# Performance work log

Hardware: AMD Instinct MI355X
Metric: run time of the kernel (lower is better)

## Reference

```python
import jax, jax.numpy as jnp
import numpy as np

B, N, D = 2, 128, 128          # batch, nodes, dim
DE = 64                        # dim_edge_refinement
H, DH = 8, 32                  # heads, per-head dim
DI = H * DH                    # dim_inner = dim * dim_head = 256
DMI = 2 * DI                   # mlp_expansion_factor * dim_inner = 512
MD = 2                         # max_degree
S = 1 + 2 * MD                 # value/edge channel groups = 5
FFD = 512                      # int(2.0 * dim * 2) for EquivariantFeedForward


def _ln(x, g, eps=1e-5):
    mu = x.mean(-1, keepdims=True)
    var = ((x - mu) ** 2).mean(-1, keepdims=True)
    return (x - mu) / jnp.sqrt(var + eps) * g


def setup_inputs() -> dict:
    key = jax.random.key(0)
    ks = iter(jax.random.split(key, 64))
    def rn(shape, scale=1.0):
        return jax.random.normal(next(ks), shape, dtype=jnp.float32) * scale
    w = 0.05
    return dict(
        h=rn((B, N, D)), x1=rn((B, N, D, 3)), x2=rn((B, N, D, 5)),
        t_ij=rn((B, N, N, D)), r1=rn((B, N, N, 3)), r2=rn((B, N, N, 5)),
        g_i=jnp.ones((D,), jnp.float32), g_j=jnp.ones((D,), jnp.float32),
        Wq=rn((D, DI), w), Wk=rn((D, DI), w),
        Wv1=rn((D, DMI), w), bv1=jnp.zeros((DMI,), jnp.float32),
        Wv2=rn((DMI, S * DI), w), bv2=jnp.zeros((S * DI,), jnp.float32),
        Wp1=rn((D, DMI), w), bp1=jnp.zeros((DMI,), jnp.float32),
        Wp2=rn((DMI, S * DI), w), bp2=jnp.zeros((S * DI,), jnp.float32),
        Wek=rn((D, S * DI), w), Wev=rn((D, S * DI), w),
        Wcomb=rn((DI, D), w),
        Wqh=rn((D, DE), w), Wk1h=rn((D, DE), w), Wk2h=rn((D, DE), w),
        Wep=rn((2 * DE, D), w), Wres=rn((D, D), w),
        P1=rn((D, D), w), P2=rn((D, D), w),
        Wf1a=rn((2 * D, FFD), w), bf1a=jnp.zeros((FFD,), jnp.float32),
        Wf2a=rn((FFD, 2 * D), w), bf2a=jnp.zeros((2 * D,), jnp.float32),
        Wf1b=rn((2 * D, FFD), w), bf1b=jnp.zeros((FFD,), jnp.float32),
        Wf2b=rn((FFD, 2 * D), w), bf2b=jnp.zeros((2 * D,), jnp.float32),
    )


def reference(h, x1, x2, t_ij, r1, r2, g_i, g_j, Wq, Wk, Wv1, bv1, Wv2, bv2,
              Wp1, bp1, Wp2, bp2, Wek, Wev, Wcomb, Wqh, Wk1h, Wk2h, Wep, Wres,
              P1, P2, Wf1a, bf1a, Wf2a, bf2a, Wf1b, bf1b, Wf2b, bf2b):
    # ---- HierarchicalTensorRefinement: per-degree inner products -> edge refresh
    q1 = jnp.einsum('bndm,de->bnem', x1, Wqh)
    q2 = jnp.einsum('bndm,de->bnem', x2, Wqh)
    k1 = jnp.einsum('bndm,de->bnem', x1, Wk1h)
    k2 = jnp.einsum('bndm,de->bnem', x2, Wk2h)
    w_ij = jnp.concatenate([
        jnp.einsum('biem,bjem->bije', q1, k1),
        jnp.einsum('biem,bjem->bije', q2, k2)], axis=-1)       # [b,n,n,2*DE]
    t = w_ij @ Wep + t_ij @ Wres                                # [b,n,n,D]
    # ---- GeometryAwareTensorAttention
    hi = _ln(h, g_i)
    hj = _ln(h, g_j)
    q = (hi @ Wq).reshape(B, N, H, DH).transpose(0, 2, 1, 3)    # bhnd
    k = (hj @ Wk).reshape(B, N, H, DH).transpose(0, 2, 1, 3)
    v = (jax.nn.silu(hj @ Wv1 + bv1) @ Wv2 + bv2).reshape(B, N, S, H, DH).transpose(0, 3, 1, 2, 4)   # bhnsd
    pv = (jax.nn.silu(hj @ Wp1 + bp1) @ Wp2 + bp2).reshape(B, N, S, H, DH).transpose(0, 3, 1, 2, 4)
    ek = jax.nn.silu(t @ Wek).reshape(B, N, N, S, H, DH).transpose(0, 4, 1, 2, 3, 5)                  # bhijsd
    ev = (t @ Wev).reshape(B, N, N, S, H, DH).transpose(0, 4, 1, 2, 3, 5)
    sim_num = jnp.einsum('bhid,bhjd->bhij', q, k)
    sim_den = jnp.einsum('bhid,bhijsd->bhis', q, ek)            # edge-keyed denominator
    attn = sim_num[..., None] / sim_den[:, :, :, None, :]       # bhijs
    sea = attn[..., None] * v[:, :, None] + ev * pv[:, :, None]  # bhijsd
    out = sea.transpose(0, 2, 3, 4, 1, 5).reshape(B, N, N, S, H * DH) @ Wcomb  # [b,i,j,S,D]
    h_sc = out[..., 0, :]              # [b,i,j,D]
    r_sc = out[..., 1:1 + MD, :]       # [b,i,j,MD,D]
    x_sc = out[..., 1 + MD:, :]        # [b,i,j,MD,D]
    h2 = h + h_sc.sum(axis=2)
    x1a = jnp.einsum('bjdm,bijd->bidm', x1, x_sc[..., 0, :]) + jnp.einsum('bijm,bijd->bidm', r1, r_sc[..., 0, :])
    x2a = jnp.einsum('bjdm,bijd->bidm', x2, x_sc[..., 1, :]) + jnp.einsum('bijm,bijd->bidm', r2, r_sc[..., 1, :])
    # ---- EquivariantFeedForward (eq 13)
    def ff_branch(xl, P, W1, b1, W2, b2):
        proj = jnp.einsum('bndm,de->bnem', xl, P)
        inv = jnp.sqrt((proj ** 2).sum(-1) + 1e-12)             # invariant norm over m
        mo = jax.nn.silu(jnp.concatenate([h2, inv], -1) @ W1 + b1) @ W2 + b2
        m1, m2 = jnp.split(mo, 2, axis=-1)
        return m1, proj * m2[..., None]
    m1a, xr1 = ff_branch(x1a, P1, Wf1a, bf1a, Wf2a, bf2a)
    m1b, xr2 = ff_branch(x2a, P2, Wf1b, bf1b, Wf2b, bf2b)
    h3 = h2 + m1a + m1b
    x1f = x1a + xr1
    x2f = x2a + xr2
    # pack outputs: h [b,n,d,1] | x1 [b,n,d,3] | x2 [b,n,d,5] -> [b,n,d,9]
    return jnp.concatenate([h3[..., None], x1f, x2f], axis=-1)
```

## Files before the change

### kernel.cpp

```cpp
#include <hip/hip_runtime.h>
#include <math.h>

#define OFF_Q    0
#define OFF_K    65536
#define OFF_A1V  131072
#define OFF_A1P  262144
#define OFF_V    393216
#define OFF_PV   720896
#define OFF_VW   1048576
#define OFF_QK   2359296
#define OFF_T    2621440
#define OFF_DEN  6815744
#define OFF_ACC  6825984
#define OFF_WEVT 7940096
#define OFF_WCT  8022016
#define OFF_HI   8038400
#define OFF_HJ   8071168

typedef __bf16 bf16x8 __attribute__((ext_vector_type(8)));
typedef float  f32x4  __attribute__((ext_vector_type(4)));

__device__ __forceinline__ float silu_f(float x){
  return x / (1.0f + __expf(-x));
}
__device__ __forceinline__ unsigned short f2bf(float x){
  union{float f; unsigned u;} c; c.f = x;
  unsigned r = c.u + 0x7FFFu + ((c.u >> 16) & 1u);
  return (unsigned short)(r >> 16);
}
__device__ __forceinline__ unsigned packbf(float a, float b){
  return (unsigned)f2bf(a) | ((unsigned)f2bf(b) << 16);
}
__device__ __forceinline__ void swz_store(float* Abase, int k, int j, float v){
  *(float*)((char*)Abase + k*256 + ((((j>>2) ^ ((k>>2)&15))) << 4) + ((j&3)<<2)) = v;
}
__device__ __forceinline__ f32x4 swz_load4(const float* Abase, int k, int chunk){
  return *(const f32x4*)((const char*)Abase + k*256 + ((chunk ^ ((k>>2)&15)) << 4));
}

__global__ __launch_bounds__(128) void k0a_ln(
    const float* __restrict__ h, const float* __restrict__ g_i, const float* __restrict__ g_j,
    float* __restrict__ ws)
{
  __shared__ float red[2];
  const int r = blockIdx.x, tid = threadIdx.x;
  const int w = tid >> 6, l = tid & 63;
  const float hv = h[r*128 + tid];
  float s = hv;
  #pragma unroll
  for (int o = 1; o < 64; o <<= 1) s += __shfl_xor(s, o);
  if (l == 0) red[w] = s;
  __syncthreads();
  const float mu = (red[0] + red[1]) * (1.f/128.f);
  const float dv = hv - mu;
  float s2 = dv*dv;
  #pragma unroll
  for (int o = 1; o < 64; o <<= 1) s2 += __shfl_xor(s2, o);
  __syncthreads();
  if (l == 0) red[w] = s2;
  __syncthreads();
  const float rstd = 1.0f / sqrtf((red[0] + red[1])*(1.f/128.f) + 1e-5f);
  ws[OFF_HI + r*128 + tid] = dv * rstd * g_i[tid];
  ws[OFF_HJ + r*128 + tid] = dv * rstd * g_j[tid];
  if (tid < 40) ws[OFF_DEN + r*40 + tid] = 0.f;
}

__global__ __launch_bounds__(256) void k0b_qkv(
    const float* __restrict__ Wq, const float* __restrict__ Wk,
    const float* __restrict__ Wv1, const float* __restrict__ bv1,
    const float* __restrict__ Wp1, const float* __restrict__ bp1,
    float* __restrict__ ws)
{
  __shared__ float hrow[128];
  const int bid = blockIdx.x;
  const int row = bid / 6, ch = bid - 6*(bid/6);
  const int tid = threadIdx.x;
  if (tid < 128) hrow[tid] = ws[((ch == 0) ? OFF_HI : OFF_HJ) + row*128 + tid];
  __syncthreads();
  const float* W; int c; float bias = 0.f; bool act = false; float* dst; int wstride;
  switch(ch){
    case 0: W = Wq;  c = tid;      wstride = 256; dst = ws + OFF_Q   + row*256 + c; break;
    case 1: W = Wk;  c = tid;      wstride = 256; dst = ws + OFF_K   + row*256 + c; break;
    case 2: W = Wv1; c = tid;      wstride = 512; bias = bv1[c]; act = true; dst = ws + OFF_A1V + row*512 + c; break;
    case 3: W = Wv1; c = 256+tid;  wstride = 512; bias = bv1[c]; act = true; dst = ws + OFF_A1V + row*512 + c; break;
    case 4: W = Wp1; c = tid;      wstride = 512; bias = bp1[c]; act = true; dst = ws + OFF_A1P + row*512 + c; break;
    default:W = Wp1; c = 256+tid;  wstride = 512; bias = bp1[c]; act = true; dst = ws + OFF_A1P + row*512 + c; break;
  }
  float acc = bias;
  #pragma unroll 8
  for (int d = 0; d < 128; ++d) acc += hrow[d] * W[d*wstride + c];
  *dst = act ? silu_f(acc) : acc;
}

__global__ __launch_bounds__(256) void k0c_qk12(
    const float* __restrict__ x1, const float* __restrict__ x2,
    const float* __restrict__ Wqh, const float* __restrict__ Wk1h, const float* __restrict__ Wk2h,
    float* __restrict__ ws)
{
  __shared__ float x1r[384], x2r[640];
  const int row = blockIdx.x, tid = threadIdx.x;
  for (int idx = tid; idx < 384; idx += 256) x1r[idx] = x1[row*384 + idx];
  for (int idx = tid; idx < 640; idx += 256) x2r[idx] = x2[row*640 + idx];
  __syncthreads();
  for (int idx = tid; idx < 512; idx += 256){
    if (idx < 192){
      const int e = idx/3, m = idx - e*3;
      float qa = 0.f, ka = 0.f;
      #pragma unroll 8
      for (int d = 0; d < 128; ++d){
        const float xv = x1r[d*3 + m];
        qa += xv*Wqh[d*64 + e];
        ka += xv*Wk1h[d*64 + e];
      }
      ws[OFF_QK + row*1024 + idx] = qa;
      ws[OFF_QK + row*1024 + 512 + idx] = ka;
    } else {
      const int i2 = idx - 192;
      const int e = i2/5, m = i2 - e*5;
      float qa = 0.f, ka = 0.f;
      #pragma unroll 8
      for (int d = 0; d < 128; ++d){
        const float xv = x2r[d*5 + m];
        qa += xv*Wqh[d*64 + e];
        ka += xv*Wk2h[d*64 + e];
      }
      ws[OFF_QK + row*1024 + 192 + i2] = qa;
      ws[OFF_QK + row*1024 + 704 + i2] = ka;
    }
  }
}

__global__ __launch_bounds__(256) void k1_vp(
    const float* __restrict__ Wv2, const float* __restrict__ bv2,
    const float* __restrict__ Wp2, const float* __restrict__ bp2,
    float* __restrict__ ws)
{
  __shared__ float A[512][16];
  __shared__ float Bc[64][128];
  const int tid = threadIdx.x;
  const int rt = blockIdx.x & 31;
  const int ct = blockIdx.x >> 5;
  const int r0 = rt*16;
  const bool isP = (r0 >= 256);
  const int rbase = isP ? (r0 - 256) : r0;
  const float* __restrict__ src  = ws + (isP ? OFF_A1P : OFF_A1V);
  const float* __restrict__ W    = isP ? Wp2 : Wv2;
  const float* __restrict__ bias = isP ? bp2 : bv2;
  const int c0 = ct*128;
  for (int idx = tid; idx < 2048; idx += 256){
    const int rl = idx & 15;
    const int c4 = (idx >> 4) * 4;
    const float4 v = *(const float4*)&src[(rbase+rl)*512 + c4];
    A[c4+0][rl] = v.x; A[c4+1][rl] = v.y; A[c4+2][rl] = v.z; A[c4+3][rl] = v.w;
  }
  float acc[4][2] = {{0.f}};
  const int rg = tid & 3;
  const int cg = tid >> 2;
  for (int kc = 0; kc < 8; ++kc){
    __syncthreads();
    for (int idx = tid; idx < 2048; idx += 256){
      const int kl = idx >> 5;
      const int c4 = (idx & 31)*4;
      *(float4*)&Bc[kl][c4] = *(const float4*)&W[(kc*64+kl)*1280 + c0 + c4];
    }
    __syncthreads();
    #pragma unroll 8
    for (int k = 0; k < 64; ++k){
      const float4 a = *(const float4*)&A[kc*64+k][rg*4];
      const float b0 = Bc[k][cg*2], b1 = Bc[k][cg*2+1];
      acc[0][0] += a.x*b0; acc[0][1] += a.x*b1;
      acc[1][0] += a.y*b0; acc[1][1] += a.y*b1;
      acc[2][0] += a.z*b0; acc[2][1] += a.z*b1;
      acc[3][0] += a.w*b0; acc[3][1] += a.w*b1;
    }
  }
  float* __restrict__ dst = ws + (isP ? OFF_PV : OFF_V);
  for (int rr = 0; rr < 4; ++rr)
    for (int cc = 0; cc < 2; ++cc){
      const int c = c0 + cg*2 + cc;
      dst[(rbase + rg*4 + rr)*1280 + c] = acc[rr][cc] + bias[c];
    }
}

__global__ __launch_bounds__(256) void k2_vw(const float* __restrict__ Wcomb, float* __restrict__ ws)
{
  __shared__ float vr[1280];
  const int j = blockIdx.x, tid = threadIdx.x;
  for (int idx = tid; idx < 320; idx += 256)
    *(float4*)&vr[idx*4] = *(const float4*)&ws[OFF_V + j*1280 + idx*4];
  __syncthreads();
  const int d = tid & 127;
  for (int sh = tid >> 7; sh < 40; sh += 2){
    const int s = sh >> 3, hh = sh & 7;
    float a = 0.f;
    #pragma unroll 8
    for (int dh = 0; dh < 32; ++dh)
      a += vr[s*256 + hh*32 + dh] * Wcomb[(hh*32+dh)*128 + d];
    ws[OFF_VW + j*5120 + sh*128 + d] = a;
  }
}

__global__ __launch_bounds__(256) void k_cvt(
    const float* __restrict__ Wev, const float* __restrict__ Wcomb, float* __restrict__ ws)
{
  __shared__ float ld[16][256];
  const int tid = threadIdx.x;
  if (blockIdx.x < 80){
    const int c0 = blockIdx.x*16;
    for (int p = 0; p < 8; ++p){
      const int idx = tid + p*256;
      const int k = idx >> 4, cl = idx & 15;
      ld[cl][k] = Wev[k*1280 + c0 + cl];
    }
    __syncthreads();
    const int cl = tid >> 4, k8 = tid & 15;
    uint4 u;
    u.x = packbf(ld[cl][k8*8+0], ld[cl][k8*8+1]);
    u.y = packbf(ld[cl][k8*8+2], ld[cl][k8*8+3]);
    u.z = packbf(ld[cl][k8*8+4], ld[cl][k8*8+5]);
    u.w = packbf(ld[cl][k8*8+6], ld[cl][k8*8+7]);
    ((uint4*)(ws + OFF_WEVT))[(c0+cl)*16 + k8] = u;
  } else {
    const int c0 = (blockIdx.x - 80)*16;
    for (int p = 0; p < 16; ++p){
      const int idx = tid + p*256;
      const int k = idx >> 4, cl = idx & 15;
      ld[cl][k] = Wcomb[k*128 + c0 + cl];
    }
    __syncthreads();
    const int cl = tid >> 4, k8i = tid & 15;
    for (int pass = 0; pass < 2; ++pass){
      const int k8 = k8i + pass*16;
      uint4 u;
      u.x = packbf(ld[cl][k8*8+0], ld[cl][k8*8+1]);
      u.y = packbf(ld[cl][k8*8+2], ld[cl][k8*8+3]);
      u.z = packbf(ld[cl][k8*8+4], ld[cl][k8*8+5]);
      u.w = packbf(ld[cl][k8*8+6], ld[cl][k8*8+7]);
      ((uint4*)(ws + OFF_WCT))[(c0+cl)*32 + k8] = u;
    }
  }
}

__global__ __launch_bounds__(512, 2) void k3_t(
    const float* __restrict__ t_ij, const float* __restrict__ Wep, const float* __restrict__ Wres,
    float* __restrict__ ws)
{
  __shared__ float A[16384];
  __shared__ float qrow[512];
  float* kst = A + 8192;
  const int tid = threadIdx.x;
  const int bi = blockIdx.x >> 1;
  const int jt = blockIdx.x & 1;
  const int j0 = jt*64;
  const int b  = bi >> 7;
  if (tid < 128) *(float4*)&qrow[tid*4] = *(const float4*)&ws[OFF_QK + bi*1024 + tid*4];
  for (int jq = 0; jq < 4; ++jq){
    __syncthreads();
    for (int idx = tid; idx < 2048; idx += 512){
      const int jl = idx & 15;
      const int c4 = (idx >> 4)*4;
      const float4 v = *(const float4*)&ws[OFF_QK + (b*128 + j0 + jq*16 + jl)*1024 + 512 + c4];
      kst[(c4+0)*16 + jl] = v.x; kst[(c4+1)*16 + jl] = v.y;
      kst[(c4+2)*16 + jl] = v.z; kst[(c4+3)*16 + jl] = v.w;
    }
    __syncthreads();
    for (int idx = tid; idx < 2048; idx += 512){
      const int jl = idx & 15;
      const int e  = idx >> 4;
      float acc = 0.f;
      if (e < 64){
        #pragma unroll
        for (int m = 0; m < 3; ++m) acc += qrow[e*3+m] * kst[(e*3+m)*16 + jl];
      } else {
        const int e2 = e - 64;
        #pragma unroll
        for (int m = 0; m < 5; ++m) acc += qrow[192 + e2*5+m] * kst[(192 + e2*5+m)*16 + jl];
      }
      swz_store(A, e, jq*16 + jl, acc);
    }
  }
  __syncthreads();
  for (int idx = tid; idx < 2048; idx += 512){
    const int jl = idx >> 5;
    const int d4 = (idx & 31)*4;
    const float4 v = *(const float4*)&t_ij[(bi*128 + j0 + jl)*128 + d4];
    swz_store(A, 128+d4+0, jl, v.x);
    swz_store(A, 128+d4+1, jl, v.y);
    swz_store(A, 128+d4+2, jl, v.z);
    swz_store(A, 128+d4+3, jl, v.w);
  }
  __syncthreads();
  const int jg = tid >> 5;
  const int cg = tid & 31;
  f32x4 acc[4] = {{0,0,0,0},{0,0,0,0},{0,0,0,0},{0,0,0,0}};
  {
    const float* Wp = Wep + cg*4;
    f32x4 wv = *(const f32x4*)Wp;
    for (int k = 0; k < 127; ++k){
      const f32x4 wn = *(const f32x4*)(Wp + (k+1)*128);
      const f32x4 av = swz_load4(A, k, jg);
      acc[0] += wv*av[0]; acc[1] += wv*av[1]; acc[2] += wv*av[2]; acc[3] += wv*av[3];
      wv = wn;
    }
    const f32x4 av = swz_load4(A, 127, jg);
    acc[0] += wv*av[0]; acc[1] += wv*av[1]; acc[2] += wv*av[2]; acc[3] += wv*av[3];
  }
  {
    const float* Wp = Wres + cg*4;
    f32x4 wv = *(const f32x4*)Wp;
    for (int k = 0; k < 127; ++k){
      const f32x4 wn = *(const f32x4*)(Wp + (k+1)*128);
      const f32x4 av = swz_load4(A, 128+k, jg);
      acc[0] += wv*av[0]; acc[1] += wv*av[1]; acc[2] += wv*av[2]; acc[3] += wv*av[3];
      wv = wn;
    }
    const f32x4 av = swz_load4(A, 255, jg);
    acc[0] += wv*av[0]; acc[1] += wv*av[1]; acc[2] += wv*av[2]; acc[3] += wv*av[3];
  }
  #pragma unroll
  for (int jj = 0; jj < 4; ++jj)
    *(f32x4*)&ws[OFF_T + (bi*128 + j0 + jg*4 + jj)*128 + cg*4] = acc[jj];
}

__global__ __launch_bounds__(256) void k4_den(
    const float* __restrict__ Wek, float* __restrict__ ws)
{
  __shared__ float tl[8192];
  __shared__ float colsum[8][128];
  __shared__ float den40[40];
  const int tid = threadIdx.x;
  const int bid = blockIdx.x;
  const int bi = bid / 20;
  const int rem = bid - bi*20;
  const int jh = rem & 1;
  const int cq = rem >> 1;
  const int j0 = jh*64;
  for (int idx = tid; idx < 2048; idx += 256){
    const int j = idx >> 5;
    const int d4 = (idx & 31)*4;
    const float4 v = *(const float4*)&ws[OFF_T + (bi*128 + j0 + j)*128 + d4];
    swz_store(tl, d4+0, j, v.x);
    swz_store(tl, d4+1, j, v.y);
    swz_store(tl, d4+2, j, v.z);
    swz_store(tl, d4+3, j, v.w);
  }
  if (tid < 40) den40[tid] = 0.f;
  __syncthreads();
  const int w = tid >> 5;
  const int lane = tid & 31;
  const float* wekp = Wek + cq*128 + lane*4;
  f32x4 acc[8];
  #pragma unroll
  for (int i = 0; i < 8; ++i) acc[i] = (f32x4){0,0,0,0};
  f32x4 wv = *(const f32x4*)wekp;
  for (int k = 0; k < 127; ++k){
    const f32x4 wn = *(const f32x4*)(wekp + (k+1)*1280);
    #pragma unroll
    for (int q = 0; q < 2; ++q){
      const f32x4 tv = swz_load4(tl, k, w*2 + q);
      acc[q*4+0] += wv*tv[0]; acc[q*4+1] += wv*tv[1];
      acc[q*4+2] += wv*tv[2]; acc[q*4+3] += wv*tv[3];
    }
    wv = wn;
  }
  #pragma unroll
  for (int q = 0; q < 2; ++q){
    const f32x4 tv = swz_load4(tl, 127, w*2 + q);
    acc[q*4+0] += wv*tv[0]; acc[q*4+1] += wv*tv[1];
    acc[q*4+2] += wv*tv[2]; acc[q*4+3] += wv*tv[3];
  }
  f32x4 cs = {0,0,0,0};
  #pragma unroll
  for (int i = 0; i < 8; ++i){
    #pragma unroll
    for (int cc = 0; cc < 4; ++cc) cs[cc] += silu_f(acc[i][cc]);
  }
  *(f32x4*)&colsum[w][lane*4] = cs;
  __syncthreads();
  if (tid < 128){
    const int c = tid;
    const float jsum = colsum[0][c] + colsum[1][c] + colsum[2][c] + colsum[3][c]
                     + colsum[4][c] + colsum[5][c] + colsum[6][c] + colsum[7][c];
    const int col = cq*128 + c;
    const int s  = col >> 8;
    const int hd = col & 255;
    atomicAdd(&den40[(hd>>5)*5 + s], jsum * ws[OFF_Q + bi*256 + hd]);
  }
  __syncthreads();
  if (tid < 40 && den40[tid] != 0.f)
    atomicAdd(&ws[OFF_DEN + bi*40 + tid], den40[tid]);
}

__global__ __launch_bounds__(512, 4) void k5_pass2(
    const float* __restrict__ x1, const float* __restrict__ x2,
    const float* __restrict__ r1, const float* __restrict__ r2,
    float* __restrict__ ws)
{
  __shared__ unsigned short tA[8192];
  __shared__ unsigned short wevB[8192];
  __shared__ unsigned short wcombB[8192];
  __shared__ unsigned short epB[4096];
  __shared__ float num[8][64];
  __shared__ float acc17[17*128];
  __shared__ float ql[256];
  __shared__ float rdenl[40];

  const int tid  = threadIdx.x;
  const int lane = tid & 63;
  const int w    = tid >> 6;
  const int wm   = w & 3;
  const int wn   = w >> 2;
  const int l15  = lane & 15;
  const int kq   = lane >> 4;

  const int bi = blockIdx.x >> 1;
  const int jh = blockIdx.x & 1;
  const int j0 = jh*64;
  const int b  = bi >> 7;

  #pragma unroll
  for (int p = 0; p < 4; ++p){
    const int idx = tid + p*512;
    const int j = idx >> 5;
    const int d4 = (idx & 31)*4;
    const float4 v = *(const float4*)&ws[OFF_T + (bi*128 + j0 + j)*128 + d4];
    uint2 u;
    u.x = packbf(v.x, v.y);
    u.y = packbf(v.z, v.w);
    *(uint2*)((char*)tA + j*256 + ((d4*2) ^ ((j&7)<<4))) = u;
  }
  if (tid < 64) *(float4*)&ql[tid*4] = *(const float4*)&ws[OFF_Q + bi*256 + tid*4];
  if (tid < 40) rdenl[tid] = 1.0f / ws[OFF_DEN + bi*40 + tid];
  for (int idx = tid; idx < 17*128; idx += 512) acc17[idx] = 0.f;
  __syncthreads();

  {
    const int hh = tid >> 6, jl = tid & 63;
    const float* krow = &ws[OFF_K + (b*128 + j0 + jl)*256 + hh*32];
    float a = 0.f;
    #pragma unroll
    for (int dh = 0; dh < 32; ++dh) a += ql[hh*32+dh]*krow[dh];
    num[hh][jl] = a;
  }

  const int jA = wm*16 + l15;
  bf16x8 af[4];
  #pragma unroll
  for (int ks = 0; ks < 4; ++ks)
    af[ks] = *(const bf16x8*)((const char*)tA + jA*256 + ((ks*64 + kq*16) ^ ((jA&7)<<4)));

  const uint4* wevt = (const uint4*)(ws + OFF_WEVT);
  const uint4* wct  = (const uint4*)(ws + OFF_WCT);

  for (int s = 0; s < 5; ++s){
    f32x4 o0 = {0,0,0,0}, o1 = {0,0,0,0}, o2 = {0,0,0,0}, o3 = {0,0,0,0};
    for (int ch4 = 0; ch4 < 4; ++ch4){
      __syncthreads();
      #pragma unroll
      for (int p = 0; p < 2; ++p){
        const int idx = tid + p*512;
        const int cl = idx & 63, kg = idx >> 6;
        const uint4 v = wevt[(s*256 + ch4*64 + cl)*16 + kg];
        *(uint4*)((char*)wevB + cl*256 + ((kg*16) ^ ((cl&7)<<4))) = v;
      }
      #pragma unroll
      for (int p = 0; p < 2; ++p){
        const int idx = tid + p*512;
        const int hg = idx & 7, d = idx >> 3;
        const uint4 v = wct[d*32 + ch4*8 + hg];
        *(uint4*)((char*)wcombB + d*128 + ((hg*16) ^ ((d&7)<<4))) = v;
      }
      __syncthreads();
      f32x4 ev0 = {0,0,0,0}, ev1 = {0,0,0,0};
      {
        const int c0l = wn*32 + l15;
        const int c1l = c0l + 16;
        #pragma unroll
        for (int ks = 0; ks < 4; ++ks){
          const bf16x8 b0 = *(const bf16x8*)((const char*)wevB + c0l*256 + ((ks*64 + kq*16) ^ ((c0l&7)<<4)));
          const bf16x8 b1 = *(const bf16x8*)((const char*)wevB + c1l*256 + ((ks*64 + kq*16) ^ ((c1l&7)<<4)));
          ev0 = __builtin_amdgcn_mfma_f32_16x16x32_bf16(af[ks], b0, ev0, 0, 0, 0);
          ev1 = __builtin_amdgcn_mfma_f32_16x16x32_bf16(af[ks], b1, ev1, 0, 0, 0);
        }
      }
      #pragma unroll
      for (int nt = 0; nt < 2; ++nt){
        const int cl = wn*32 + nt*16 + l15;
        const int cglob = s*256 + ch4*64 + cl;
        #pragma unroll
        for (int r = 0; r < 4; ++r){
          const int jl = wm*16 + kq*4 + r;
          const float pvv = ws[OFF_PV + (b*128 + j0 + jl)*1280 + cglob];
          const float evv = (nt == 0) ? ev0[r] : ev1[r];
          *(unsigned short*)((char*)epB + jl*128 + ((cl*2) ^ ((jl&7)<<4))) = f2bf(evv * pvv);
        }
      }
      __syncthreads();
      #pragma unroll
      for (int ks = 0; ks < 2; ++ks){
        const bf16x8 a = *(const bf16x8*)((const char*)epB + jA*128 + ((ks*64 + kq*16) ^ ((jA&7)<<4)));
        #pragma unroll
        for (int nt = 0; nt < 4; ++nt){
          const int dl = wn*64 + nt*16 + l15;
          const bf16x8 bb = *(const bf16x8*)((const char*)wcombB + dl*128 + ((ks*64 + kq*16) ^ ((dl&7)<<4)));
          if      (nt == 0) o0 = __builtin_amdgcn_mfma_f32_16x16x32_bf16(a, bb, o0, 0, 0, 0);
          else if (nt == 1) o1 = __builtin_amdgcn_mfma_f32_16x16x32_bf16(a, bb, o1, 0, 0, 0);
          else if (nt == 2) o2 = __builtin_amdgcn_mfma_f32_16x16x32_bf16(a, bb, o2, 0, 0, 0);
          else              o3 = __builtin_amdgcn_mfma_f32_16x16x32_bf16(a, bb, o3, 0, 0, 0);
        }
      }
    }
    #pragma unroll
    for (int r = 0; r < 4; ++r){
      const int jl = wm*16 + kq*4 + r;
      const float* vwbase = ws + OFF_VW + (b*128 + j0 + jl)*5120 + s*1024 + wn*64 + l15;
      #pragma unroll
      for (int hh = 0; hh < 8; ++hh){
        const float at = num[hh][jl] * rdenl[hh*5 + s];
        const float* vp = vwbase + hh*128;
        o0[r] += at * vp[0];
        o1[r] += at * vp[16];
        o2[r] += at * vp[32];
        o3[r] += at * vp[48];
      }
    }
    if (s == 0){
      #pragma unroll
      for (int nt = 0; nt < 4; ++nt){
        const f32x4 oo = (nt==0)?o0:(nt==1)?o1:(nt==2)?o2:o3;
        float p = oo[0] + oo[1] + oo[2] + oo[3];
        p += __shfl_xor(p, 16);
        p += __shfl_xor(p, 32);
        if (lane < 16) atomicAdd(&acc17[wn*64 + nt*16 + lane], p);
      }
    } else if (s <= 2){
      const int M = (s == 1) ? 3 : 5;
      const int slot0 = (s == 1) ? 1 : 4;
      const float* rw = (s == 1) ? r1 : r2;
      for (int m = 0; m < M; ++m){
        float wj[4];
        #pragma unroll
        for (int r = 0; r < 4; ++r)
          wj[r] = rw[(bi*128 + j0 + wm*16 + kq*4 + r)*M + m];
        #pragma unroll
        for (int nt = 0; nt < 4; ++nt){
          const f32x4 oo = (nt==0)?o0:(nt==1)?o1:(nt==2)?o2:o3;
          float p = wj[0]*oo[0] + wj[1]*oo[1] + wj[2]*oo[2] + wj[3]*oo[3];
          p += __shfl_xor(p, 16);
          p += __shfl_xor(p, 32);
          if (lane < 16) atomicAdd(&acc17[(slot0+m)*128 + wn*64 + nt*16 + lane], p);
        }
      }
    } else {
      const int M = (s == 3) ? 3 : 5;
      const int slot0 = (s == 3) ? 9 : 12;
      const float* xw = (s == 3) ? x1 : x2;
      for (int m = 0; m < M; ++m){
        #pragma unroll
        for (int nt = 0; nt < 4; ++nt){
          const int d = wn*64 + nt*16 + l15;
          const f32x4 oo = (nt==0)?o0:(nt==1)?o1:(nt==2)?o2:o3;
          float p = 0.f;
          #pragma unroll
          for (int r = 0; r < 4; ++r)
            p += xw[((b*128 + j0 + wm*16 + kq*4 + r)*128 + d)*M + m] * oo[r];
          p += __shfl_xor(p, 16);
          p += __shfl_xor(p, 32);
          if (lane < 16) atomicAdd(&acc17[(slot0+m)*128 + d], p);
        }
      }
    }
  }
  __syncthreads();
  for (int idx = tid; idx < 2176; idx += 512)
    ws[OFF_ACC + (bi*2 + jh)*2176 + idx] = acc17[idx];
}

__global__ __launch_bounds__(256) void k6_tail(
    const float* __restrict__ h,
    const float* __restrict__ P1, const float* __restrict__ P2,
    const float* __restrict__ Wf1a, const float* __restrict__ bf1a,
    const float* __restrict__ Wf2a, const float* __restrict__ bf2a,
    const float* __restrict__ Wf1b, const float* __restrict__ bf1b,
    const float* __restrict__ Wf2b, const float* __restrict__ bf2b,
    const float* __restrict__ ws, float* __restrict__ out)
{
  __shared__ float a17[2176];
  __shared__ float h2s[128];
  __shared__ float x1a[384], x2a[640];
  __shared__ float pj1[384], pj2[640];
  __shared__ float inv1[128], inv2[128];
  __shared__ float za[512], zb[512];
  __shared__ float m1a[128], m2a[128], m1b[128], m2b[128];
  const int tid = threadIdx.x;
  const int row = blockIdx.x;
  for (int idx = tid; idx < 2176; idx += 256)
    a17[idx] = ws[OFF_ACC + (row*2)*2176 + idx] + ws[OFF_ACC + (row*2+1)*2176 + idx];
  __syncthreads();
  if (tid < 128) h2s[tid] = h[row*128 + tid] + a17[tid];
  for (int idx = tid; idx < 384; idx += 256){
    const int d = idx/3, m = idx - d*3;
    x1a[idx] = a17[(1+m)*128 + d] + a17[(9+m)*128 + d];
  }
  for (int idx = tid; idx < 640; idx += 256){
    const int d = idx/5, m = idx - d*5;
    x2a[idx] = a17[(4+m)*128 + d] + a17[(12+m)*128 + d];
  }
  __syncthreads();
  if (tid < 128){
    const int e = tid;
    float pa[3] = {0.f,0.f,0.f};
    for (int d = 0; d < 128; ++d){
      const float p = P1[d*128 + e];
      pa[0] += x1a[d*3+0]*p;
      pa[1] += x1a[d*3+1]*p;
      pa[2] += x1a[d*3+2]*p;
    }
    pj1[e*3+0] = pa[0]; pj1[e*3+1] = pa[1]; pj1[e*3+2] = pa[2];
    inv1[e] = sqrtf(pa[0]*pa[0] + pa[1]*pa[1] + pa[2]*pa[2] + 1e-12f);
  } else {
    const int e = tid - 128;
    float pa[5] = {0.f,0.f,0.f,0.f,0.f};
    for (int d = 0; d < 128; ++d){
      const float p = P2[d*128 + e];
      pa[0] += x2a[d*5+0]*p;
      pa[1] += x2a[d*5+1]*p;
      pa[2] += x2a[d*5+2]*p;
      pa[3] += x2a[d*5+3]*p;
      pa[4] += x2a[d*5+4]*p;
    }
    #pragma unroll
    for (int m = 0; m < 5; ++m) pj2[e*5+m] = pa[m];
    inv2[e] = sqrtf(pa[0]*pa[0]+pa[1]*pa[1]+pa[2]*pa[2]+pa[3]*pa[3]+pa[4]*pa[4] + 1e-12f);
  }
  __syncthreads();
  for (int it = 0; it < 2; ++it){
    const int f = tid + it*256;
    float av = bf1a[f], bv_ = bf1b[f];
    #pragma unroll 4
    for (int k = 0; k < 128; ++k){
      av  += h2s[k]*Wf1a[k*512 + f];
      bv_ += h2s[k]*Wf1b[k*512 + f];
    }
    #pragma unroll 4
    for (int k = 0; k < 128; ++k){
      av  += inv1[k]*Wf1a[(128+k)*512 + f];
      bv_ += inv2[k]*Wf1b[(128+k)*512 + f];
    }
    za[f] = silu_f(av); zb[f] = silu_f(bv_);
  }
  __syncthreads();
  {
    const int g = tid;
    float am = bf2a[g], bm = bf2b[g];
    #pragma unroll 4
    for (int f = 0; f < 512; ++f){
      am += za[f]*Wf2a[f*256 + g];
      bm += zb[f]*Wf2b[f*256 + g];
    }
    if (g < 128){ m1a[g] = am; m1b[g] = bm; }
    else        { m2a[g-128] = am; m2b[g-128] = bm; }
  }
  __syncthreads();
  if (tid < 128){
    const int d = tid;
    const int ob = (row*128 + d)*9;
    out[ob+0] = h2s[d] + m1a[d] + m1b[d];
    #pragma unroll
    for (int m = 0; m < 3; ++m)
      out[ob+1+m] = x1a[d*3+m] + pj1[d*3+m]*m2a[d];
    #pragma unroll
    for (int m = 0; m < 5; ++m)
      out[ob+4+m] = x2a[d*5+m] + pj2[d*5+m]*m2b[d];
  }
}

extern "C" void kernel_launch(void* const* d_in, const int* in_sizes, int n_in,
                              void* d_out, int out_size, void* d_ws, size_t ws_size,
                              hipStream_t stream)
{
  (void)in_sizes; (void)n_in; (void)out_size; (void)ws_size;
  const float* h    = (const float*)d_in[0];
  const float* x1   = (const float*)d_in[1];
  const float* x2   = (const float*)d_in[2];
  const float* t_ij = (const float*)d_in[3];
  const float* r1   = (const float*)d_in[4];
  const float* r2   = (const float*)d_in[5];
  const float* g_i  = (const float*)d_in[6];
  const float* g_j  = (const float*)d_in[7];
  const float* Wq   = (const float*)d_in[8];
  const float* Wk   = (const float*)d_in[9];
  const float* Wv1  = (const float*)d_in[10];
  const float* bv1  = (const float*)d_in[11];
  const float* Wv2  = (const float*)d_in[12];
  const float* bv2  = (const float*)d_in[13];
  const float* Wp1  = (const float*)d_in[14];
  const float* bp1  = (const float*)d_in[15];
  const float* Wp2  = (const float*)d_in[16];
  const float* bp2  = (const float*)d_in[17];
  const float* Wek  = (const float*)d_in[18];
  const float* Wev  = (const float*)d_in[19];
  const float* Wcomb= (const float*)d_in[20];
  const float* Wqh  = (const float*)d_in[21];
  const float* Wk1h = (const float*)d_in[22];
  const float* Wk2h = (const float*)d_in[23];
  const float* Wep  = (const float*)d_in[24];
  const float* Wres = (const float*)d_in[25];
  const float* P1   = (const float*)d_in[26];
  const float* P2   = (const float*)d_in[27];
  const float* Wf1a = (const float*)d_in[28];
  const float* bf1a = (const float*)d_in[29];
  const float* Wf2a = (const float*)d_in[30];
  const float* bf2a = (const float*)d_in[31];
  const float* Wf1b = (const float*)d_in[32];
  const float* bf1b = (const float*)d_in[33];
  const float* Wf2b = (const float*)d_in[34];
  const float* bf2b = (const float*)d_in[35];
  float* ws  = (float*)d_ws;
  float* out = (float*)d_out;

  k0a_ln <<<dim3(256),  dim3(128), 0, stream>>>(h, g_i, g_j, ws);
  k0b_qkv<<<dim3(1536), dim3(256), 0, stream>>>(Wq, Wk, Wv1, bv1, Wp1, bp1, ws);
  k0c_qk12<<<dim3(256), dim3(256), 0, stream>>>(x1, x2, Wqh, Wk1h, Wk2h, ws);
  k1_vp  <<<dim3(320),  dim3(256), 0, stream>>>(Wv2, bv2, Wp2, bp2, ws);
  k2_vw  <<<dim3(256),  dim3(256), 0, stream>>>(Wcomb, ws);
  k_cvt  <<<dim3(88),   dim3(256), 0, stream>>>(Wev, Wcomb, ws);
  k3_t   <<<dim3(512),  dim3(512), 0, stream>>>(t_ij, Wep, Wres, ws);
  k4_den <<<dim3(5120), dim3(256), 0, stream>>>(Wek, ws);
  k5_pass2<<<dim3(512), dim3(512), 0, stream>>>(x1, x2, r1, r2, ws);
  k6_tail<<<dim3(256),  dim3(256), 0, stream>>>(h, P1, P2, Wf1a, bf1a, Wf2a, bf2a, Wf1b, bf1b, Wf2b, bf2b, ws, out);
}
```

Before: 702.1 us.

## Load MFMA operands directly from global memory and double-buffer epB in k5_pass2

k5_pass2 no longer stages t_ij, Wev^T and Wcomb^T tiles in LDS. A fragments are loaded and packed to bf16 straight from global memory into registers, and B fragments are read directly from the global bf16 weight buffers. The epB scratch is double-buffered so one barrier per chunk can be dropped, and the occupancy hint in launch_bounds is removed. This cuts LDS use and synchronisation, but depends on L1/L2 serving repeated, less coalesced global weight reads in place of LDS reuse.

Result: slower. 717.5 us (+2.2%).

```diff
diff --git a/kernel.cpp b/kernel.cpp
--- a/kernel.cpp
+++ b/kernel.cpp
@@ -391,15 +391,12 @@
     atomicAdd(&ws[OFF_DEN + bi*40 + tid], den40[tid]);
 }
 
-__global__ __launch_bounds__(512, 4) void k5_pass2(
+__global__ __launch_bounds__(512) void k5_pass2(
     const float* __restrict__ x1, const float* __restrict__ x2,
     const float* __restrict__ r1, const float* __restrict__ r2,
     float* __restrict__ ws)
 {
-  __shared__ unsigned short tA[8192];
-  __shared__ unsigned short wevB[8192];
-  __shared__ unsigned short wcombB[8192];
-  __shared__ unsigned short epB[4096];
+  __shared__ unsigned short epB[2][4096];
   __shared__ float num[8][64];
   __shared__ float acc17[17*128];
   __shared__ float ql[256];
@@ -418,20 +415,22 @@
   const int j0 = jh*64;
   const int b  = bi >> 7;
 
-  #pragma unroll
-  for (int p = 0; p < 4; ++p){
-    const int idx = tid + p*512;
-    const int j = idx >> 5;
-    const int d4 = (idx & 31)*4;
-    const float4 v = *(const float4*)&ws[OFF_T + (bi*128 + j0 + j)*128 + d4];
-    uint2 u;
-    u.x = packbf(v.x, v.y);
-    u.y = packbf(v.z, v.w);
-    *(uint2*)((char*)tA + j*256 + ((d4*2) ^ ((j&7)<<4))) = u;
-  }
   if (tid < 64) *(float4*)&ql[tid*4] = *(const float4*)&ws[OFF_Q + bi*256 + tid*4];
   if (tid < 40) rdenl[tid] = 1.0f / ws[OFF_DEN + bi*40 + tid];
   for (int idx = tid; idx < 17*128; idx += 512) acc17[idx] = 0.f;
+
+  const int jA = wm*16 + l15;
+  union { bf16x8 v; uint4 q; } afu[4];
+  #pragma unroll
+  for (int ks = 0; ks < 4; ++ks){
+    const float* tp = &ws[OFF_T + (bi*128 + j0 + jA)*128 + ks*32 + kq*8];
+    const float4 t0 = *(const float4*)tp;
+    const float4 t1 = *(const float4*)(tp + 4);
+    afu[ks].q.x = packbf(t0.x, t0.y);
+    afu[ks].q.y = packbf(t0.z, t0.w);
+    afu[ks].q.z = packbf(t1.x, t1.y);
+    afu[ks].q.w = packbf(t1.z, t1.w);
+  }
   __syncthreads();
 
   {
@@ -443,72 +442,53 @@
     num[hh][jl] = a;
   }
 
-  const int jA = wm*16 + l15;
-  bf16x8 af[4];
-  #pragma unroll
-  for (int ks = 0; ks < 4; ++ks)
-    af[ks] = *(const bf16x8*)((const char*)tA + jA*256 + ((ks*64 + kq*16) ^ ((jA&7)<<4)));
-
-  const uint4* wevt = (const uint4*)(ws + OFF_WEVT);
-  const uint4* wct  = (const uint4*)(ws + OFF_WCT);
-
+  const __bf16* wevt = (const __bf16*)(ws + OFF_WEVT);
+  const __bf16* wct  = (const __bf16*)(ws + OFF_WCT);
+
+  int pb = 0;
   for (int s = 0; s < 5; ++s){
     f32x4 o0 = {0,0,0,0}, o1 = {0,0,0,0}, o2 = {0,0,0,0}, o3 = {0,0,0,0};
     for (int ch4 = 0; ch4 < 4; ++ch4){
-      __syncthreads();
-      #pragma unroll
-      for (int p = 0; p < 2; ++p){
-        const int idx = tid + p*512;
-        const int cl = idx & 63, kg = idx >> 6;
-        const uint4 v = wevt[(s*256 + ch4*64 + cl)*16 + kg];
-        *(uint4*)((char*)wevB + cl*256 + ((kg*16) ^ ((cl&7)<<4))) = v;
-      }
-      #pragma unroll
-      for (int p = 0; p < 2; ++p){
-        const int idx = tid + p*512;
-        const int hg = idx & 7, d = idx >> 3;
-        const uint4 v = wct[d*32 + ch4*8 + hg];
-        *(uint4*)((char*)wcombB + d*128 + ((hg*16) ^ ((d&7)<<4))) = v;
-      }
-      __syncthreads();
+      const int cb = s*256 + ch4*64;
       f32x4 ev0 = {0,0,0,0}, ev1 = {0,0,0,0};
       {
         const int c0l = wn*32 + l15;
         const int c1l = c0l + 16;
         #pragma unroll
         for (int ks = 0; ks < 4; ++ks){
-          const bf16x8 b0 = *(const bf16x8*)((const char*)wevB + c0l*256 + ((ks*64 + kq*16) ^ ((c0l&7)<<4)));
-          const bf16x8 b1 = *(const bf16x8*)((const char*)wevB + c1l*256 + ((ks*64 + kq*16) ^ ((c1l&7)<<4)));
-          ev0 = __builtin_amdgcn_mfma_f32_16x16x32_bf16(af[ks], b0, ev0, 0, 0, 0);
-          ev1 = __builtin_amdgcn_mfma_f32_16x16x32_bf16(af[ks], b1, ev1, 0, 0, 0);
+          const bf16x8 b0 = *(const bf16x8*)(wevt + (cb + c0l)*128 + ks*32 + kq*8);
+          const bf16x8 b1 = *(const bf16x8*)(wevt + (cb + c1l)*128 + ks*32 + kq*8);
+          ev0 = __builtin_amdgcn_mfma_f32_16x16x32_bf16(afu[ks].v, b0, ev0, 0, 0, 0);
+          ev1 = __builtin_amdgcn_mfma_f32_16x16x32_bf16(afu[ks].v, b1, ev1, 0, 0, 0);
         }
       }
       #pragma unroll
       for (int nt = 0; nt < 2; ++nt){
         const int cl = wn*32 + nt*16 + l15;
-        const int cglob = s*256 + ch4*64 + cl;
+        const int cglob = cb + cl;
         #pragma unroll
         for (int r = 0; r < 4; ++r){
           const int jl = wm*16 + kq*4 + r;
           const float pvv = ws[OFF_PV + (b*128 + j0 + jl)*1280 + cglob];
           const float evv = (nt == 0) ? ev0[r] : ev1[r];
-          *(unsigned short*)((char*)epB + jl*128 + ((cl*2) ^ ((jl&7)<<4))) = f2bf(evv * pvv);
+          *(unsigned short*)((char*)epB[pb] + jl*128 + ((cl*2) ^ ((jl&7)<<4))) = f2bf(evv * pvv);
         }
       }
       __syncthreads();
       #pragma unroll
       for (int ks = 0; ks < 2; ++ks){
-        const bf16x8 a = *(const bf16x8*)((const char*)epB + jA*128 + ((ks*64 + kq*16) ^ ((jA&7)<<4)));
+        const bf16x8 a = *(const bf16x8*)((const char*)epB[pb] + jA*128 + ((ks*64 + kq*16) ^ ((jA&7)<<4)));
         #pragma unroll
         for (int nt = 0; nt < 4; ++nt){
           const int dl = wn*64 + nt*16 + l15;
-          const bf16x8 bb = *(const bf16x8*)((const char*)wcombB + dl*128 + ((ks*64 + kq*16) ^ ((dl&7)<<4)));
+          const bf16x8 bb = *(const bf16x8*)(wct + dl*256 + ch4*64 + ks*32 + kq*8);
           if      (nt == 0) o0 = __builtin_amdgcn_mfma_f32_16x16x32_bf16(a, bb, o0, 0, 0, 0);
           else if (nt == 1) o1 = __builtin_amdgcn_mfma_f32_16x16x32_bf16(a, bb, o1, 0, 0, 0);
           else if (nt == 2) o2 = __builtin_amdgcn_mfma_f32_16x16x32_bf16(a, bb, o2, 0, 0, 0);
           else              o3 = __builtin_amdgcn_mfma_f32_16x16x32_bf16(a, bb, o3, 0, 0, 0);
         }
       }
+      pb ^= 1;
     }
     #pragma unroll
     for (int r = 0; r < 4; ++r){
```
